# Kernel optimization log

Hardware: AMD Instinct MI355X
Metric: run time of the kernel (lower is better)

The kernel has to match this reference:

```python
import jax, jax.numpy as jnp
import numpy as np
from jax.scipy.special import logsumexp

# ---- static hyperparameters (from init_kwargs) ----
NG, NF, NW = 5, 10, 4
STEP = NG + NF + 1            # 16 signatures per writer mini-batch
T, D_FEAT = 512, 64           # sequence length, embedding dim
N = NW * STEP                 # 64 sequences in the batch
GAMMA = 5.0                   # soft-DTW gamma (bandwidth=0.1 -> int 0 -> no band)
MARGIN, ALPHA, BETA = 1.0, 0.1, 1.0
P_W, R_W = 0.1, 0.1
K_NUM, K_MUL = 5, 2.0
BIG = 1e10                    # stand-in for +inf in the DP boundary


def setup_inputs() -> dict:
    key = jax.random.key(0)
    k1, k2 = jax.random.split(key)
    data = jax.random.normal(k1, (N, T, D_FEAT), dtype=jnp.float32)
    lens = jax.random.randint(k2, (N,), T // 2, T + 1).astype(jnp.int32)
    return {"data": data, "lens": lens}


def _softdtw_batch(A, B, la, lb):
    """Batched soft-DTW (squared-Euclidean cost, softmin with gamma).
    A, B: (P, T, d); la, lb: (P,) int lengths. Returns R[la, lb] per pair.
    Anti-diagonal wavefront scan: diagonal k holds R[i, k-i]."""
    P = A.shape[0]
    a2 = jnp.sum(A * A, -1)
    b2 = jnp.sum(B * B, -1)
    Dm = a2[:, :, None] + b2[:, None, :] - 2.0 * jnp.einsum('ptd,psd->pts', A, B)  # (P,T,T)
    i_idx = jnp.arange(T + 1)
    r0 = jnp.broadcast_to(jnp.where(i_idx == 0, 0.0, BIG), (P, T + 1))  # diag k=0: R[0,0]=0
    r1 = jnp.full((P, T + 1), BIG, dtype=A.dtype)                        # diag k=1: boundary inf

    def shift(x):  # x[i] -> x[i-1], pad row i=0 with BIG
        return jnp.concatenate([jnp.full((P, 1), BIG, x.dtype), x[:, :-1]], axis=1)

    def step(carry, k):
        p2, p1 = carry          # diagonals k-2, k-1, each (P, T+1) indexed by i
        j = k - i_idx
        valid = (i_idx >= 1) & (j >= 1) & (j <= T)
        di = jnp.clip(i_idx - 1, 0, T - 1)
        dj = jnp.clip(j - 1, 0, T - 1)
        cost = Dm[:, di, dj]    # (P, T+1)
        # softmin over (R[i-1,j-1], R[i-1,j], R[i,j-1])
        stack = jnp.stack([shift(p2), shift(p1), p1], 0)
        smin = -GAMMA * logsumexp(-stack / GAMMA, axis=0)
        cur = jnp.where(valid[None, :], cost + smin, BIG)
        return (p1, cur), cur

    ks = jnp.arange(2, 2 * T + 1)
    _, ys = jax.lax.scan(step, (r0, r1), ks)  # (2T-1, P, T+1)
    return ys[la + lb - 2, jnp.arange(P), la]


def _mmd_pair(X, Y):
    """Multi-kernel Gaussian MMD between X, Y: (n, F) each."""
    n = X.shape[0]
    total = jnp.concatenate([X, Y], 0)
    sq = jnp.sum(total * total, -1)
    L2 = sq[:, None] + sq[None, :] - 2.0 * total @ total.T
    m = total.shape[0]
    bw = jnp.sum(L2) / (m * m - m)
    bw = bw / (K_MUL ** (K_NUM // 2))
    bws = bw * (K_MUL ** jnp.arange(K_NUM, dtype=X.dtype))
    K = jnp.sum(jnp.exp(-L2[None, :, :] / bws[:, None, None]), 0)
    return (jnp.mean(K[:n, :n]) + jnp.mean(K[n:, n:])
            - jnp.mean(K[:n, n:]) - jnp.mean(K[n:, :n]))


def _forward(data, lens):
    half = NF // 2
    # all anchor/(positive|negative) pairs across writers, flattened: P = NW*(NG+NF)
    a_idx, b_idx = [], []
    for w in range(NW):
        base = w * STEP
        for j in range(1, STEP):
            a_idx.append(base)
            b_idx.append(base + j)
    a_idx = jnp.array(a_idx)
    b_idx = jnp.array(b_idx)
    la, lb = lens[a_idx], lens[b_idx]
    raw = _softdtw_batch(data[a_idx], data[b_idx], la, lb)
    dist = (raw / (la + lb).astype(data.dtype)).reshape(NW, NG + NF)
    dist_g, dist_n = dist[:, :NG], dist[:, NG:]
    dk = jnp.sqrt(jnp.abs(jnp.mean(dist_g, 1)))       # (NW,)
    dg = dist_g / dk[:, None]
    dn = dist_n / dk[:, None]
    lk_s = jax.nn.relu(dg[:, :, None] + MARGIN - dn[:, None, :half])
    lk_r = jax.nn.relu(dg[:, :, None] + MARGIN - dn[:, None, half:])
    ca = jnp.mean(dg, 1)
    cb = jnp.mean(dn[:, :half], 1)
    intra = jnp.sum(dg - ca[:, None], 1)
    inter = jax.nn.relu(BETA - jnp.abs(ca - cb))
    cnt = jax.lax.stop_gradient(
        (jnp.sum(lk_s > 0, (1, 2)) + jnp.sum(lk_r > 0, (1, 2))).astype(data.dtype))
    lv = (jnp.sum(lk_s, (1, 2)) + jnp.sum(lk_r, (1, 2))) / (cnt + 1.0)
    total_loss = jnp.mean(lv + intra * P_W + inter * R_W)

    # pairwise MMD over writer mini-batches (first 1+NG+half signatures each)
    src, tgt = [], []
    for i in range(NW):
        for j in range(1, NW):
            if i != j:
                src.append(np.arange(STEP * i, STEP * (i + 1) - half))
                tgt.append(np.arange(STEP * j, STEP * (j + 1) - half))
    src = jnp.array(np.stack(src))
    tgt = jnp.array(np.stack(tgt))
    Xs = data[src].reshape(src.shape[0], src.shape[1], -1)  # flatten (T,d) per signature
    Ys = data[tgt].reshape(tgt.shape[0], tgt.shape[1], -1)
    mmds = jax.vmap(_mmd_pair)(Xs, Ys)
    siz = NW * (NW + 1) // 2
    mmds = jnp.concatenate([mmds, jnp.zeros(siz - mmds.shape[0], data.dtype)])
    return total_loss + jnp.max(mmds) * ALPHA


def reference(data, lens):
    return _forward(data, lens)
```

## Files before the change

### kernel.cpp

```cpp
#include <hip/hip_runtime.h>
#include <cstdint>
#include <cstddef>

#define TT 512
#define DFEAT 64
#define NPAIR 60
#define INV_GLN2 0.28853900817779268f
#define NEG_GLN2 -3.4657359027997265f
#define NEGE (-(1 << 29))
#define BM 128
#define BK 64

__constant__ int d_WI[9] = {0,0,0,1,1,2,2,3,3};
__constant__ int d_WJ[9] = {1,2,3,2,3,1,3,1,2};

#if __has_builtin(__builtin_amdgcn_exp2f)
__device__ __forceinline__ float fexp2(float x) { return __builtin_amdgcn_exp2f(x); }
#else
__device__ __forceinline__ float fexp2(float x) { return __expf(0.6931471805599453f * x); }
#endif
#if __has_builtin(__builtin_amdgcn_logf)
__device__ __forceinline__ float flog2(float x) { return __builtin_amdgcn_logf(x); }
#else
__device__ __forceinline__ float flog2(float x) { return 1.4426950408889634f * __logf(x); }
#endif
#if __has_builtin(__builtin_amdgcn_ldexpf)
__device__ __forceinline__ float fldexp(float x, int n) { return __builtin_amdgcn_ldexpf(x, n); }
#else
__device__ __forceinline__ float fldexp(float x, int n) { return ldexpf(x, n); }
#endif
#if __has_builtin(__builtin_amdgcn_frexp_mantf)
__device__ __forceinline__ float fmant(float x) { return __builtin_amdgcn_frexp_mantf(x); }
#else
__device__ __forceinline__ float fmant(float x) { int e; return frexpf(x, &e); }
#endif
#if __has_builtin(__builtin_amdgcn_frexp_expf)
__device__ __forceinline__ int fexpo(float x) { return __builtin_amdgcn_frexp_expf(x); }
#else
__device__ __forceinline__ int fexpo(float x) { int e; frexpf(x, &e); return e; }
#endif

__device__ __forceinline__ unsigned short f2bf(float f) {
  unsigned u = __float_as_uint(f);
  unsigned r = (u + 0x7FFFu + ((u >> 16) & 1u)) >> 16;
  return (unsigned short)r;
}

__global__ __launch_bounds__(256) void norms_kernel(const float* __restrict__ data,
                                                    float* __restrict__ norms) {
  const int g = blockIdx.x * 256 + threadIdx.x;
  const float* __restrict__ row = data + (size_t)g * DFEAT;
  float s = 0.f;
#pragma unroll
  for (int k = 0; k < DFEAT; k += 4) {
    float4 v = *(const float4*)(row + k);
    s += v.x * v.x + v.y * v.y + v.z * v.z + v.w * v.w;
  }
  norms[g] = s;
}

__global__ __launch_bounds__(256) void cost_kernel(const float* __restrict__ data,
                                                   const float* __restrict__ norms,
                                                   const int* __restrict__ lens,
                                                   unsigned short* __restrict__ Dm) {
  const int p = blockIdx.z;
  const int w = p / 15, jb = p % 15 + 1;
  const int la = lens[w * 16], lb = lens[w * 16 + jb];
  const int i0 = blockIdx.y * BM, j0 = blockIdx.x * BM;
  if (i0 >= la || j0 >= lb) return;
  const int an = w * 16, bn = w * 16 + jb;
  const float* __restrict__ A = data + (size_t)an * (TT * DFEAT);
  const float* __restrict__ B = data + (size_t)bn * (TT * DFEAT);

  __shared__ float smem[2 * BK * BM];
  float* As = smem;
  float* Bs = smem + BK * BM;

  const int tid = threadIdx.x;
#pragma unroll
  for (int s2 = 0; s2 < 8; ++s2) {
    const int f = tid + s2 * 256;
    const int row = f >> 4;
    const int k4 = (f & 15) << 2;
    float4 va = *(const float4*)(A + (size_t)(i0 + row) * DFEAT + k4);
    float4 vb = *(const float4*)(B + (size_t)(j0 + row) * DFEAT + k4);
#pragma unroll
    for (int q = 0; q < 4; ++q) {
      const int k = k4 + q;
      const int cp = row ^ (k & 24);
      As[k * BM + cp] = ((const float*)&va)[q];
      Bs[k * BM + cp] = ((const float*)&vb)[q];
    }
  }
  const int ty = tid >> 4, tx = tid & 15;
  const int r0 = ty * 8, c0 = tx * 8;
  float aI[8], bI[8];
#pragma unroll
  for (int q = 0; q < 8; ++q) {
    aI[q] = norms[(size_t)an * TT + i0 + r0 + q] * INV_GLN2;
    bI[q] = norms[(size_t)bn * TT + j0 + c0 + q] * INV_GLN2;
  }
  __syncthreads();

  float acc[8][8] = {};
#pragma unroll 4
  for (int k = 0; k < BK; ++k) {
    const int v = k & 24;
    float af[8], bf8[8];
    *(float4*)&af[0] = *(const float4*)&As[k * BM + (r0 ^ v)];
    *(float4*)&af[4] = *(const float4*)&As[k * BM + (r0 ^ v) + 4];
    *(float4*)&bf8[0] = *(const float4*)&Bs[k * BM + (c0 ^ v)];
    *(float4*)&bf8[4] = *(const float4*)&Bs[k * BM + (c0 ^ v) + 4];
#pragma unroll
    for (int r = 0; r < 8; ++r)
#pragma unroll
      for (int cc = 0; cc < 8; ++cc)
        acc[r][cc] += af[r] * bf8[cc];
  }
  __syncthreads();

  unsigned short* wst = (unsigned short*)smem;
  const float twoInv = 2.0f * INV_GLN2;
#pragma unroll
  for (int cc = 0; cc < 8; ++cc) {
    const int col = c0 + cc;
    unsigned short t8[8];
#pragma unroll
    for (int r = 0; r < 8; ++r) {
      const float x = twoInv * acc[r][cc] - aI[r] - bI[cc];
      t8[r] = f2bf(fexp2(x));
    }
    const int G = ty * 128 + col;
    const int Gs = G ^ (tx & 7);
    const unsigned u0 = (unsigned)t8[0] | ((unsigned)t8[1] << 16);
    const unsigned u1 = (unsigned)t8[2] | ((unsigned)t8[3] << 16);
    const unsigned u2 = (unsigned)t8[4] | ((unsigned)t8[5] << 16);
    const unsigned u3 = (unsigned)t8[6] | ((unsigned)t8[7] << 16);
    uint4 vv; vv.x = u0; vv.y = u1; vv.z = u2; vv.w = u3;
    *(uint4*)&wst[Gs * 8] = vv;
  }
  __syncthreads();
  unsigned short* __restrict__ Dp = Dm + (size_t)p * (TT * TT);
#pragma unroll
  for (int s2 = 0; s2 < 8; ++s2) {
    const int g = tid + s2 * 256;
    const int band = g >> 7, col = g & 127;
    const int Gs = g ^ ((col >> 3) & 7);
    uint4 vv = *(const uint4*)&wst[Gs * 8];
    *(uint4*)(Dp + (size_t)((i0 >> 3) + band) * (TT * 8) + (size_t)(j0 + col) * 8) = vv;
  }
}

__global__ __launch_bounds__(256) void dpgram_kernel(const unsigned short* __restrict__ Dm,
                                                     const int* __restrict__ lens,
                                                     float* __restrict__ raw,
                                                     const float* __restrict__ data,
                                                     float* __restrict__ partials) {
  __shared__ float X[44][516];
  if (blockIdx.x < NPAIR) {
    if (threadIdx.x >= 64) return;
    const int p = blockIdx.x;
    const int w = p / 15, jb = p % 15 + 1;
    const int la = lens[w * 16];
    const int lb = lens[w * 16 + jb];
    const int t = threadIdx.x;
    const int L = (la - 1) >> 3;
    const int dsel = (la - 1) & 7;
    const int s_end = lb + L;

    const unsigned short* __restrict__ base =
        Dm + (size_t)p * (TT * TT) + (size_t)t * (TT * 8);

    float Xm[8]; int Xe[8];
#pragma unroll
    for (int d = 0; d < 8; ++d) { Xm[d] = 0.f; Xe[d] = NEGE; }
    float upAm = (t == 0) ? 0.5f : 0.f;
    int   upAe = (t == 0) ? 1 : NEGE;
    float upBm = 0.f;
    int   upBe = NEGE;

    auto colidx = [&](int sigma) { return min(max(sigma - t - 1, 0), TT - 1); };
    auto ldcol = [&](int cc) { return *(const uint4*)(base + (size_t)cc * 8); };

    uint4 ring[8];
#pragma unroll
    for (int j = 0; j < 8; ++j) ring[j] = ldcol(colidx(1 + j));

    int s = 1;
    while (s <= s_end) {
#pragma unroll
      for (int j = 0; j < 8; ++j) {
        if (s <= s_end) {
          float W8[8];
          {
            const unsigned u[4] = {ring[j].x, ring[j].y, ring[j].z, ring[j].w};
#pragma unroll
            for (int i = 0; i < 4; ++i) {
              W8[2 * i]     = __uint_as_float(u[i] << 16);
              W8[2 * i + 1] = __uint_as_float(u[i] & 0xFFFF0000u);
            }
          }
          ring[j] = ldcol(colidx(s + 8));
          const int c = s - t;
          if (c >= 1 && c <= TT) {
            float Am = upAm; int Ae = upAe;
            float Bm = upBm; int Be = upBe;
#pragma unroll
            for (int d = 0; d < 8; ++d) {
              const float Cm = Xm[d]; const int Ce = Xe[d];
              const int em = max(max(Ae, Be), Ce);
              const float sum = fldexp(Am, Ae - em) + fldexp(Cm, Ce - em) +
                                fldexp(Bm, Be - em);
              const float pr = W8[d] * sum;
              const float nm = fmant(pr);
              const int ne = em + fexpo(pr);
              Am = Cm; Ae = Ce;
              Bm = nm; Be = ne;
              Xm[d] = nm; Xe[d] = ne;
            }
          }
          const float shm = __shfl_up(Xm[7], 1);
          const int she = __shfl_up(Xe[7], 1);
          upAm = upBm; upAe = upBe;
          upBm = (t == 0) ? 0.f : shm;
          upBe = (t == 0) ? NEGE : she;
          ++s;
        }
      }
    }

    if (t == L) {
      float xm = Xm[0]; int xe = Xe[0];
#pragma unroll
      for (int d = 1; d < 8; ++d)
        if (dsel == d) { xm = Xm[d]; xe = Xe[d]; }
      raw[p] = NEG_GLN2 * ((float)xe + flog2(xm));
    }
  } else {
    const int c = blockIdx.x - NPAIR;
    const int tid = threadIdx.x;
#pragma unroll
    for (int s = 0; s < 22; ++s) {
      const int f = tid + s * 256;
      const int r = f >> 7;
      const int c4 = (f & 127) << 2;
      const int n = (r / 11) * 16 + (r % 11);
      float4 v = *(const float4*)(data + (size_t)n * (TT * DFEAT) + c * 512 + c4);
      X[r][c4 + 0] = v.x; X[r][c4 + 1] = v.y; X[r][c4 + 2] = v.z; X[r][c4 + 3] = v.w;
    }
    __syncthreads();
    for (int e = tid; e < 44 * 44; e += 256) {
      const int ii = e / 44, jj = e % 44;
      const float* xi = &X[ii][0];
      const float* xj = &X[jj][0];
      float acc = 0.f;
#pragma unroll 8
      for (int k = 0; k < 512; k += 4) {
        float4 u = *(const float4*)(xi + k);
        float4 v = *(const float4*)(xj + k);
        acc += u.x * v.x + u.y * v.y + u.z * v.z + u.w * v.w;
      }
      partials[(size_t)c * (44 * 44) + e] = acc;
    }
  }
}

__device__ __forceinline__ float blockReduceSum(float v, float* sred) {
#pragma unroll
  for (int off = 32; off > 0; off >>= 1) v += __shfl_down(v, off);
  const int tid = threadIdx.x;
  if ((tid & 63) == 0) sred[tid >> 6] = v;
  __syncthreads();
  const float r = sred[0] + sred[1] + sred[2] + sred[3];
  __syncthreads();
  return r;
}

__global__ __launch_bounds__(256) void final_kernel(const float* __restrict__ partials,
                                                    const float* __restrict__ raw,
                                                    const int* __restrict__ lens,
                                                    float* __restrict__ out) {
  __shared__ float G[44 * 44];
  __shared__ float sred[4];
  const int tid = threadIdx.x;
  for (int e = tid; e < 44 * 44; e += 256) {
    float s = 0.f;
    for (int cc = 0; cc < 64; ++cc) s += partials[(size_t)cc * (44 * 44) + e];
    G[e] = s;
  }
  __syncthreads();
  float maxm = 0.f;
  for (int pp = 0; pp < 9; ++pp) {
    const int wi = d_WI[pp], wj = d_WJ[pp];
    float part = 0.f;
    for (int e = tid; e < 484; e += 256) {
      const int p = e / 22, q = e % 22;
      const int vp = (p < 11) ? (wi * 11 + p) : (wj * 11 + p - 11);
      const int vq = (q < 11) ? (wi * 11 + q) : (wj * 11 + q - 11);
      part += G[vp * 44 + vp] + G[vq * 44 + vq] - 2.f * G[vp * 44 + vq];
    }
    const float suml2 = blockReduceSum(part, sred);
    const float bw = suml2 / 462.0f * 0.25f;
    float aXX = 0.f, aXY = 0.f, aYX = 0.f, aYY = 0.f;
    for (int e = tid; e < 484; e += 256) {
      const int p = e / 22, q = e % 22;
      const int vp = (p < 11) ? (wi * 11 + p) : (wj * 11 + p - 11);
      const int vq = (q < 11) ? (wi * 11 + q) : (wj * 11 + q - 11);
      const float l2 = G[vp * 44 + vp] + G[vq * 44 + vq] - 2.f * G[vp * 44 + vq];
      float kk = 0.f;
      float inv = 1.0f / bw;
#pragma unroll
      for (int tkr = 0; tkr < 5; ++tkr) { kk += __expf(-l2 * inv); inv *= 0.5f; }
      const bool pl = p < 11, ql = q < 11;
      aXX += (pl && ql) ? kk : 0.f;
      aXY += (pl && !ql) ? kk : 0.f;
      aYX += (!pl && ql) ? kk : 0.f;
      aYY += (!pl && !ql) ? kk : 0.f;
    }
    const float sXX = blockReduceSum(aXX, sred);
    const float sXY = blockReduceSum(aXY, sred);
    const float sYX = blockReduceSum(aYX, sred);
    const float sYY = blockReduceSum(aYY, sred);
    if (tid == 0) {
      const float mmd = (sXX + sYY - sXY - sYX) / 121.f;
      maxm = fmaxf(maxm, mmd);
    }
  }
  if (tid == 0) {
    float total = 0.f;
    for (int w = 0; w < 4; ++w) {
      const int la0 = lens[w * 16];
      float dist[15];
      for (int q = 0; q < 15; ++q) {
        const int lb = lens[w * 16 + q + 1];
        dist[q] = raw[w * 15 + q] / (float)(la0 + lb);
      }
      const float mg = (dist[0] + dist[1] + dist[2] + dist[3] + dist[4]) * 0.2f;
      const float dk = sqrtf(fabsf(mg));
      float dg[5], dn[10];
      for (int q = 0; q < 5; ++q) dg[q] = dist[q] / dk;
      for (int q = 0; q < 10; ++q) dn[q] = dist[5 + q] / dk;
      float lsum = 0.f, cnt = 0.f;
      for (int a = 0; a < 5; ++a)
        for (int b = 0; b < 10; ++b) {
          const float v = dg[a] + 1.0f - dn[b];
          if (v > 0.f) { lsum += v; cnt += 1.f; }
        }
      const float ca = (dg[0] + dg[1] + dg[2] + dg[3] + dg[4]) * 0.2f;
      const float cb = (dn[0] + dn[1] + dn[2] + dn[3] + dn[4]) * 0.2f;
      float intra = 0.f;
      for (int q = 0; q < 5; ++q) intra += dg[q] - ca;
      const float inter = fmaxf(1.0f - fabsf(ca - cb), 0.f);
      total += lsum / (cnt + 1.0f) + 0.1f * intra + 0.1f * inter;
    }
    total *= 0.25f;
    out[0] = total + 0.1f * maxm;
  }
}

extern "C" void kernel_launch(void* const* d_in, const int* in_sizes, int n_in,
                              void* d_out, int out_size, void* d_ws, size_t ws_size,
                              hipStream_t stream) {
  const float* data = (const float*)d_in[0];
  const int* lens = (const int*)d_in[1];
  float* out = (float*)d_out;
  char* ws = (char*)d_ws;

  const size_t DMB = (size_t)NPAIR * TT * TT * sizeof(unsigned short);
  const size_t RAWB = 1024;
  const size_t PARTB = (size_t)64 * 44 * 44 * sizeof(float);

  unsigned short* Dm = (unsigned short*)ws;
  float* raw = (float*)(ws + DMB);
  float* partials = (float*)(ws + DMB + RAWB);
  float* norms = (float*)(ws + DMB + RAWB + PARTB);

  norms_kernel<<<128, 256, 0, stream>>>(data, norms);
  cost_kernel<<<dim3(4, 4, NPAIR), 256, 0, stream>>>(data, norms, lens, Dm);
  dpgram_kernel<<<NPAIR + 64, 256, 0, stream>>>(Dm, lens, raw, data, partials);
  final_kernel<<<1, 256, 0, stream>>>(partials, raw, lens, out);
}
```

Baseline: 320.0 us.

## Split DP and Gram kernels, transpose cost layout, shorten DP critical path

The cost matrix is now stored column-major by band, so the 64 DP lanes read one contiguous 1KB column per step instead of strided 8KB-apart chunks. The fused dpgram kernel is split into a 64-thread DP kernel and a separate Gram kernel. The DP recurrence now precomputes the diagonal/left partial sums before the serial dependency on the up-neighbour, which shortens the per-cell dependency chain. The main loop also drops its per-step bounds check, handling the tail separately. Launching the Gram kernel afterward serializes work that previously ran concurrently in one grid.

```diff
diff --git a/kernel.cpp b/kernel.cpp
--- a/kernel.cpp
+++ b/kernel.cpp
@@ -130,138 +130,154 @@
       const float x = twoInv * acc[r][cc] - aI[r] - bI[cc];
       t8[r] = f2bf(fexp2(x));
     }
-    const int G = ty * 128 + col;
-    const int Gs = G ^ (tx & 7);
     const unsigned u0 = (unsigned)t8[0] | ((unsigned)t8[1] << 16);
     const unsigned u1 = (unsigned)t8[2] | ((unsigned)t8[3] << 16);
     const unsigned u2 = (unsigned)t8[4] | ((unsigned)t8[5] << 16);
     const unsigned u3 = (unsigned)t8[6] | ((unsigned)t8[7] << 16);
     uint4 vv; vv.x = u0; vv.y = u1; vv.z = u2; vv.w = u3;
-    *(uint4*)&wst[Gs * 8] = vv;
+    *(uint4*)&wst[(col * 16 + ty) * 8] = vv;
   }
   __syncthreads();
   unsigned short* __restrict__ Dp = Dm + (size_t)p * (TT * TT);
+  const int band0 = i0 >> 3;
 #pragma unroll
   for (int s2 = 0; s2 < 8; ++s2) {
     const int g = tid + s2 * 256;
-    const int band = g >> 7, col = g & 127;
-    const int Gs = g ^ ((col >> 3) & 7);
-    uint4 vv = *(const uint4*)&wst[Gs * 8];
-    *(uint4*)(Dp + (size_t)((i0 >> 3) + band) * (TT * 8) + (size_t)(j0 + col) * 8) = vv;
-  }
-}
-
-__global__ __launch_bounds__(256) void dpgram_kernel(const unsigned short* __restrict__ Dm,
-                                                     const int* __restrict__ lens,
-                                                     float* __restrict__ raw,
-                                                     const float* __restrict__ data,
-                                                     float* __restrict__ partials) {
+    const int col_l = g >> 4, band_l = g & 15;
+    uint4 vv = *(const uint4*)&wst[g * 8];
+    *(uint4*)(Dp + (size_t)(j0 + col_l) * 512 + (size_t)(band0 + band_l) * 8) = vv;
+  }
+}
+
+__global__ __launch_bounds__(64) void dp_kernel(const unsigned short* __restrict__ Dm,
+                                                const int* __restrict__ lens,
+                                                float* __restrict__ raw) {
+  const int p = blockIdx.x;
+  const int w = p / 15, jb = p % 15 + 1;
+  const int la = lens[w * 16];
+  const int lb = lens[w * 16 + jb];
+  const int t = threadIdx.x;
+  const int L = (la - 1) >> 3;
+  const int dsel = (la - 1) & 7;
+  const int s_end = lb + L;
+
+  const unsigned short* __restrict__ base = Dm + (size_t)p * (TT * TT) + t * 8;
+
+  float Xm[8]; int Xe[8];
+#pragma unroll
+  for (int d = 0; d < 8; ++d) { Xm[d] = 0.f; Xe[d] = NEGE; }
+  float upAm = (t == 0) ? 0.5f : 0.f;
+  int   upAe = (t == 0) ? 1 : NEGE;
+  float upBm = 0.f;
+  int   upBe = NEGE;
+
+  auto colidx = [&](int sigma) { return min(max(sigma - t - 1, 0), TT - 1); };
+  auto ldcol = [&](int cc) { return *(const uint4*)(base + (size_t)cc * 512); };
+
+  auto decode8 = [](const uint4& q, float* o) {
+    const unsigned u[4] = {q.x, q.y, q.z, q.w};
+#pragma unroll
+    for (int i = 0; i < 4; ++i) {
+      o[2 * i]     = __uint_as_float(u[i] << 16);
+      o[2 * i + 1] = __uint_as_float(u[i] & 0xFFFF0000u);
+    }
+  };
+
+  auto STEP = [&](int sigma, const float* W8) {
+    float preSm[8]; int preE[8];
+    {
+      float Am = upAm; int Ae = upAe;
+#pragma unroll
+      for (int d = 0; d < 8; ++d) {
+        const float Cm = Xm[d]; const int Ce = Xe[d];
+        const int pe = max(Ae, Ce);
+        preSm[d] = fldexp(Am, Ae - pe) + fldexp(Cm, Ce - pe);
+        preE[d] = pe;
+        Am = Cm; Ae = Ce;
+      }
+    }
+    const int c = sigma - t;
+    if (c >= 1 && c <= TT) {
+      float Bm = upBm; int Be = upBe;
+#pragma unroll
+      for (int d = 0; d < 8; ++d) {
+        const int em = max(preE[d], Be);
+        const float sum = fldexp(preSm[d], preE[d] - em) + fldexp(Bm, Be - em);
+        const float pr = W8[d] * sum;
+        const float nm = fmant(pr);
+        const int ne = em + fexpo(pr);
+        Bm = nm; Be = ne;
+        Xm[d] = nm; Xe[d] = ne;
+      }
+    }
+    const float shm = __shfl_up(Xm[7], 1);
+    const int she = __shfl_up(Xe[7], 1);
+    upAm = upBm; upAe = upBe;
+    upBm = (t == 0) ? 0.f : shm;
+    upBe = (t == 0) ? NEGE : she;
+  };
+
+  uint4 ring[8];
+#pragma unroll
+  for (int j = 0; j < 8; ++j) ring[j] = ldcol(colidx(1 + j));
+
+  int s = 1;
+  for (; s + 7 <= s_end; ) {
+#pragma unroll
+    for (int j = 0; j < 8; ++j) {
+      float W8[8];
+      decode8(ring[j], W8);
+      ring[j] = ldcol(colidx(s + 8));
+      STEP(s, W8);
+      ++s;
+    }
+  }
+#pragma unroll
+  for (int j = 0; j < 8; ++j) {
+    if (s <= s_end) {
+      float W8[8];
+      decode8(ring[j], W8);
+      STEP(s, W8);
+      ++s;
+    }
+  }
+
+  if (t == L) {
+    float xm = Xm[0]; int xe = Xe[0];
+#pragma unroll
+    for (int d = 1; d < 8; ++d)
+      if (dsel == d) { xm = Xm[d]; xe = Xe[d]; }
+    raw[p] = NEG_GLN2 * ((float)xe + flog2(xm));
+  }
+}
+
+__global__ __launch_bounds__(256) void gram_kernel(const float* __restrict__ data,
+                                                   float* __restrict__ partials) {
+  const int c = blockIdx.x;
   __shared__ float X[44][516];
-  if (blockIdx.x < NPAIR) {
-    if (threadIdx.x >= 64) return;
-    const int p = blockIdx.x;
-    const int w = p / 15, jb = p % 15 + 1;
-    const int la = lens[w * 16];
-    const int lb = lens[w * 16 + jb];
-    const int t = threadIdx.x;
-    const int L = (la - 1) >> 3;
-    const int dsel = (la - 1) & 7;
-    const int s_end = lb + L;
-
-    const unsigned short* __restrict__ base =
-        Dm + (size_t)p * (TT * TT) + (size_t)t * (TT * 8);
-
-    float Xm[8]; int Xe[8];
-#pragma unroll
-    for (int d = 0; d < 8; ++d) { Xm[d] = 0.f; Xe[d] = NEGE; }
-    float upAm = (t == 0) ? 0.5f : 0.f;
-    int   upAe = (t == 0) ? 1 : NEGE;
-    float upBm = 0.f;
-    int   upBe = NEGE;
-
-    auto colidx = [&](int sigma) { return min(max(sigma - t - 1, 0), TT - 1); };
-    auto ldcol = [&](int cc) { return *(const uint4*)(base + (size_t)cc * 8); };
-
-    uint4 ring[8];
-#pragma unroll
-    for (int j = 0; j < 8; ++j) ring[j] = ldcol(colidx(1 + j));
-
-    int s = 1;
-    while (s <= s_end) {
-#pragma unroll
-      for (int j = 0; j < 8; ++j) {
-        if (s <= s_end) {
-          float W8[8];
-          {
-            const unsigned u[4] = {ring[j].x, ring[j].y, ring[j].z, ring[j].w};
-#pragma unroll
-            for (int i = 0; i < 4; ++i) {
-              W8[2 * i]     = __uint_as_float(u[i] << 16);
-              W8[2 * i + 1] = __uint_as_float(u[i] & 0xFFFF0000u);
-            }
-          }
-          ring[j] = ldcol(colidx(s + 8));
-          const int c = s - t;
-          if (c >= 1 && c <= TT) {
-            float Am = upAm; int Ae = upAe;
-            float Bm = upBm; int Be = upBe;
-#pragma unroll
-            for (int d = 0; d < 8; ++d) {
-              const float Cm = Xm[d]; const int Ce = Xe[d];
-              const int em = max(max(Ae, Be), Ce);
-              const float sum = fldexp(Am, Ae - em) + fldexp(Cm, Ce - em) +
-                                fldexp(Bm, Be - em);
-              const float pr = W8[d] * sum;
-              const float nm = fmant(pr);
-              const int ne = em + fexpo(pr);
-              Am = Cm; Ae = Ce;
-              Bm = nm; Be = ne;
-              Xm[d] = nm; Xe[d] = ne;
-            }
-          }
-          const float shm = __shfl_up(Xm[7], 1);
-          const int she = __shfl_up(Xe[7], 1);
-          upAm = upBm; upAe = upBe;
-          upBm = (t == 0) ? 0.f : shm;
-          upBe = (t == 0) ? NEGE : she;
-          ++s;
-        }
-      }
-    }
-
-    if (t == L) {
-      float xm = Xm[0]; int xe = Xe[0];
-#pragma unroll
-      for (int d = 1; d < 8; ++d)
-        if (dsel == d) { xm = Xm[d]; xe = Xe[d]; }
-      raw[p] = NEG_GLN2 * ((float)xe + flog2(xm));
-    }
-  } else {
-    const int c = blockIdx.x - NPAIR;
-    const int tid = threadIdx.x;
-#pragma unroll
-    for (int s = 0; s < 22; ++s) {
-      const int f = tid + s * 256;
-      const int r = f >> 7;
-      const int c4 = (f & 127) << 2;
-      const int n = (r / 11) * 16 + (r % 11);
-      float4 v = *(const float4*)(data + (size_t)n * (TT * DFEAT) + c * 512 + c4);
-      X[r][c4 + 0] = v.x; X[r][c4 + 1] = v.y; X[r][c4 + 2] = v.z; X[r][c4 + 3] = v.w;
-    }
-    __syncthreads();
-    for (int e = tid; e < 44 * 44; e += 256) {
-      const int ii = e / 44, jj = e % 44;
-      const float* xi = &X[ii][0];
-      const float* xj = &X[jj][0];
-      float acc = 0.f;
+  const int tid = threadIdx.x;
+#pragma unroll
+  for (int s = 0; s < 22; ++s) {
+    const int f = tid + s * 256;
+    const int r = f >> 7;
+    const int c4 = (f & 127) << 2;
+    const int n = (r / 11) * 16 + (r % 11);
+    float4 v = *(const float4*)(data + (size_t)n * (TT * DFEAT) + c * 512 + c4);
+    X[r][c4 + 0] = v.x; X[r][c4 + 1] = v.y; X[r][c4 + 2] = v.z; X[r][c4 + 3] = v.w;
+  }
+  __syncthreads();
+  for (int e = tid; e < 44 * 44; e += 256) {
+    const int ii = e / 44, jj = e % 44;
+    const float* xi = &X[ii][0];
+    const float* xj = &X[jj][0];
+    float acc = 0.f;
 #pragma unroll 8
-      for (int k = 0; k < 512; k += 4) {
-        float4 u = *(const float4*)(xi + k);
-        float4 v = *(const float4*)(xj + k);
-        acc += u.x * v.x + u.y * v.y + u.z * v.z + u.w * v.w;
-      }
-      partials[(size_t)c * (44 * 44) + e] = acc;
-    }
+    for (int k = 0; k < 512; k += 4) {
+      float4 u = *(const float4*)(xi + k);
+      float4 v = *(const float4*)(xj + k);
+      acc += u.x * v.x + u.y * v.y + u.z * v.z + u.w * v.w;
+    }
+    partials[(size_t)c * (44 * 44) + e] = acc;
   }
 }
 
@@ -377,6 +393,7 @@
 
   norms_kernel<<<128, 256, 0, stream>>>(data, norms);
   cost_kernel<<<dim3(4, 4, NPAIR), 256, 0, stream>>>(data, norms, lens, Dm);
-  dpgram_kernel<<<NPAIR + 64, 256, 0, stream>>>(Dm, lens, raw, data, partials);
+  dp_kernel<<<NPAIR, 64, 0, stream>>>(Dm, lens, raw);
+  gram_kernel<<<64, 256, 0, stream>>>(data, partials);
   final_kernel<<<1, 256, 0, stream>>>(partials, raw, lens, out);
 }
```

Result: no change. 324.8 us (+1.5%).
